# Kernel tuning notes

Hardware: AMD Instinct MI355X
Metric: run time of the kernel (lower is better)

Reference implementation:

```python
import jax, jax.numpy as jnp
import numpy as np

NEG_SLOPE = 0.2  # PyG GATConv default negative_slope


def gat_conv(x, edge_index, W, a_src, a_dst, b):
    """PyG GATConv with add_self_loops=True, concat=False (mean over heads).
    x: [N, F_in]; W: [F_in, H*D]; a_src/a_dst: [H, D]; b: [D].
    Returns [N, D].
    """
    N = x.shape[0]
    H, D = a_src.shape
    xh = (x @ W).reshape(N, H, D)            # [N, H, D]
    loop = jnp.arange(N, dtype=edge_index.dtype)
    src = jnp.concatenate([edge_index[0], loop])  # [E+N]
    dst = jnp.concatenate([edge_index[1], loop])  # [E+N]
    # per-node attention logits
    asrc = jnp.einsum('nhd,hd->nh', xh, a_src)    # [N, H]
    adst = jnp.einsum('nhd,hd->nh', xh, a_dst)    # [N, H]
    e = asrc[src] + adst[dst]                      # [E+N, H]
    e = jnp.where(e > 0, e, NEG_SLOPE * e)         # LeakyReLU
    # softmax over incoming edges of each destination node
    emax = jax.ops.segment_max(e, dst, num_segments=N)   # [N, H]
    ex = jnp.exp(e - emax[dst])
    denom = jax.ops.segment_sum(ex, dst, num_segments=N) # [N, H]
    alpha = ex / denom[dst]                               # [E+N, H]
    # scatter-aggregate messages
    out = jax.ops.segment_sum(alpha[:, :, None] * xh[src], dst, num_segments=N)  # [N, H, D]
    return out.mean(axis=1) + b                           # concat=False -> mean heads


def setup_inputs() -> dict:
    key = jax.random.key(0)
    ks = jax.random.split(key, 10)
    N, F, D, C, H, E = 100000, 128, 32, 16, 8, 1600000
    s1 = 1.0 / np.sqrt(F)
    s2 = 1.0 / np.sqrt(D)
    return {
        'x': jax.random.normal(ks[0], (N, F), dtype=jnp.float32),
        'edge_index': jax.random.randint(ks[1], (2, E), 0, N, dtype=jnp.int32),
        'W1': jax.random.normal(ks[2], (F, H * D), dtype=jnp.float32) * s1,
        'a_src1': jax.random.normal(ks[3], (H, D), dtype=jnp.float32) * s2,
        'a_dst1': jax.random.normal(ks[4], (H, D), dtype=jnp.float32) * s2,
        'b1': jnp.zeros((D,), dtype=jnp.float32),
        'W2': jax.random.normal(ks[5], (D, H * C), dtype=jnp.float32) * s2,
        'a_src2': jax.random.normal(ks[6], (H, C), dtype=jnp.float32) * (1.0 / np.sqrt(C)),
        'a_dst2': jax.random.normal(ks[7], (H, C), dtype=jnp.float32) * (1.0 / np.sqrt(C)),
        'b2': jnp.zeros((C,), dtype=jnp.float32),
    }


def reference(x, edge_index, W1, a_src1, a_dst1, b1, W2, a_src2, a_dst2, b2):
    h = gat_conv(x, edge_index, W1, a_src1, a_dst1, b1)
    h = jax.nn.elu(h)                       # F.elu; Dropout(p=0.0) is identity
    logits = gat_conv(h, edge_index, W2, a_src2, a_dst2, b2)
    return (jax.nn.log_softmax(logits, axis=1), logits)
```

## Files before the change

### kernel.cpp

```cpp
#include <hip/hip_runtime.h>
#include <hip/hip_bf16.h>
#include <hip/hip_fp16.h>
#include <math.h>

#define LEAK 0.2f
#define BSTRIDE 64
#define NPB 128
#define CAPB 4096

typedef _Float16 f16;
typedef _Float16 f16x8 __attribute__((ext_vector_type(8)));
typedef float f32x2 __attribute__((ext_vector_type(2)));
typedef float f32x4 __attribute__((ext_vector_type(4)));

__global__ void transpose_w_k(const float* __restrict__ W, f16* __restrict__ Wt,
                              int K, int NC) {
  int idx = blockIdx.x * 256 + threadIdx.x;
  if (idx >= K * NC) return;
  int n = idx / K, k = idx - n * K;
  Wt[idx] = (f16)W[(size_t)k * NC + n];
}

__global__ __launch_bounds__(256) void binscatter_k(const int* __restrict__ ei, int E,
                                                    int Nn,
                                                    unsigned* __restrict__ binCnt,
                                                    uint2* __restrict__ recs, int NB) {
  __shared__ unsigned lh[1024];
  __shared__ unsigned gbase[1024];
  const int Mtot = E + Nn;
  for (int i = threadIdx.x; i < NB; i += 256) lh[i] = 0;
  __syncthreads();
  const int base = blockIdx.x * 4096;
  int sr[16], dr[16];
#pragma unroll
  for (int j = 0; j < 16; ++j) {
    int p = base + j * 256 + threadIdx.x;
    if (p < Mtot) {
      int ss, dd;
      if (p < E) {
        ss = ei[p];
        dd = ei[E + p];
      } else {
        ss = dd = p - E;
      }
      sr[j] = ss;
      dr[j] = dd;
      atomicAdd(&lh[dd >> 7], 1u);
    } else {
      dr[j] = -1;
      sr[j] = 0;
    }
  }
  __syncthreads();
  for (int i = threadIdx.x; i < NB; i += 256) {
    unsigned c = lh[i];
    gbase[i] = c ? atomicAdd(&binCnt[i], c) : 0u;
    lh[i] = 0;
  }
  __syncthreads();
#pragma unroll
  for (int j = 0; j < 16; ++j) {
    if (dr[j] >= 0) {
      int b = dr[j] >> 7;
      unsigned pos = gbase[b] + atomicAdd(&lh[b], 1u);
      if (pos < CAPB)
        recs[((size_t)b << 12) + pos] = make_uint2((unsigned)sr[j], (unsigned)dr[j]);
    }
  }
}

__global__ __launch_bounds__(256) void binbuild_k(const uint2* __restrict__ recs,
                                                  const unsigned* __restrict__ binCnt,
                                                  unsigned* __restrict__ cnt,
                                                  unsigned* __restrict__ bucket, int N) {
  __shared__ unsigned lcnt[NPB];
  __shared__ unsigned lbkt[NPB * BSTRIDE];
  const int b = blockIdx.x;
  for (int i = threadIdx.x; i < NPB; i += 256) lcnt[i] = 0;
  __syncthreads();
  unsigned nrec = binCnt[b];
  nrec = nrec > CAPB ? CAPB : nrec;
  const unsigned r0 = (unsigned)b << 12;
  const unsigned r1 = r0 + nrec;
  for (unsigned p = r0 + threadIdx.x; p < r1; p += 256) {
    uint2 r = recs[p];
    unsigned dl = r.y & (NPB - 1);
    unsigned pos = atomicAdd(&lcnt[dl], 1u);
    if (pos < BSTRIDE) lbkt[(dl << 6) + pos] = r.x;
  }
  __syncthreads();
  const int n0 = b * NPB;
  const int nv = (N - n0) < NPB ? (N - n0) : NPB;
  for (int i = threadIdx.x; i < nv; i += 256) cnt[n0 + i] = lcnt[i];
  uint4* gb = (uint4*)(bucket + ((size_t)n0 << 6));
  const uint4* lb = (const uint4*)lbkt;
  const int lim = nv * (BSTRIDE / 4);
  for (int i = threadIdx.x; i < lim; i += 256) gb[i] = lb[i];
}

template <int K, int BN, int DH>
__global__ __launch_bounds__(256) void gemm_att_mfma_k(
    const float* __restrict__ A, const f16* __restrict__ Bt,
    unsigned char* __restrict__ Cout, const float* __restrict__ a_src,
    const float* __restrict__ a_dst, float* __restrict__ asrc,
    float* __restrict__ adst, int M, int NC) {
  constexpr int CH = K / 8;
  constexpr int CT = BN / 16;
  constexpr int KT = K / 32;
  constexpr int LDSB = (BN * K * 2) > (64 * BN) ? (BN * K * 2) : (64 * BN);
  __shared__ __align__(16) unsigned char smem[LDSB];
  f16* Bs = (f16*)smem;
  unsigned char* stage = smem;
  const int tid = threadIdx.x;
  const int row0 = blockIdx.y * 64;
  const int col0 = blockIdx.x * BN;

#pragma unroll
  for (int it = 0; it < (BN * CH) / 256; ++it) {
    int idx = it * 256 + tid;
    int n = idx / CH, c = idx - n * CH;
    f16x8 h = *(const f16x8*)(Bt + (size_t)(col0 + n) * K + c * 8);
    *(f16x8*)&Bs[n * K + (((c + n) & (CH - 1)) << 3)] = h;
  }

  const int wv = tid >> 6;
  const int lane = tid & 63;
  const int l16 = lane & 15;
  const int l4 = lane >> 4;

  const int arow = row0 + wv * 16 + l16;
  const bool aok = arow < M;
  f16x8 afrag[KT];
#pragma unroll
  for (int kt = 0; kt < KT; ++kt) {
    float4 v0 = make_float4(0.f, 0.f, 0.f, 0.f), v1 = v0;
    if (aok) {
      const float* gp = A + (size_t)arow * K + (kt * 4 + l4) * 8;
      v0 = *(const float4*)gp;
      v1 = *(const float4*)(gp + 4);
    }
    afrag[kt] = {(f16)v0.x, (f16)v0.y, (f16)v0.z, (f16)v0.w,
                 (f16)v1.x, (f16)v1.y, (f16)v1.z, (f16)v1.w};
  }
  __syncthreads();

  f32x4 acc[CT];
#pragma unroll
  for (int ct = 0; ct < CT; ++ct) acc[ct] = (f32x4){0.f, 0.f, 0.f, 0.f};

#pragma unroll
  for (int kt = 0; kt < KT; ++kt) {
    int aj = kt * 4 + l4;
#pragma unroll
    for (int ct = 0; ct < CT; ++ct) {
      int br = ct * 16 + l16;
      f16x8 bv = *(const f16x8*)&Bs[br * K + (((aj + br) & (CH - 1)) << 3)];
      acc[ct] = __builtin_amdgcn_mfma_f32_16x16x32_f16(afrag[kt], bv, acc[ct], 0, 0, 0);
    }
  }

  constexpr int HPB = BN / DH;
  constexpr int CTH = DH / 16;
  float ps[HPB][4], pd[HPB][4];
#pragma unroll
  for (int hl = 0; hl < HPB; ++hl)
#pragma unroll
    for (int r = 0; r < 4; ++r) { ps[hl][r] = 0.f; pd[hl][r] = 0.f; }

#pragma unroll
  for (int ct = 0; ct < CT; ++ct) {
    int col = col0 + ct * 16 + l16;
    float vs = a_src[col];
    float vd = a_dst[col];
    int hl = ct / CTH;
#pragma unroll
    for (int r = 0; r < 4; ++r) {
      ps[hl][r] += acc[ct][r] * vs;
      pd[hl][r] += acc[ct][r] * vd;
    }
  }

#pragma unroll
  for (int hl = 0; hl < HPB; ++hl) {
#pragma unroll
    for (int r = 0; r < 4; ++r) {
      float s = ps[hl][r], d = pd[hl][r];
#pragma unroll
      for (int m = 1; m < 16; m <<= 1) {
        s += __shfl_xor(s, m, 64);
        d += __shfl_xor(d, m, 64);
      }
      if (l16 == 0) {
        int grow = row0 + wv * 16 + l4 * 4 + r;
        int h = (col0 / DH) + hl;
        if (grow < M) {
          asrc[(size_t)grow * 8 + h] = s;
          adst[(size_t)grow * 8 + h] = d;
        }
      }
    }
  }

  __syncthreads();
  {
    const int j = lane & 3;
    const unsigned selAB = ((4u + j) << (8 * j)) | ((unsigned)j << (8 * (j ^ 1)));
    const unsigned selCD = ((4u + j) << (8 * (j ^ 2))) | ((unsigned)j << (8 * (j ^ 3)));
    const unsigned selMix =
        0x03020100u + (0x04040404u & ((j & 2) ? 0xFFFF0000u : 0x0000FFFFu));
    const int row = wv * 16 + l4 * 4 + j;
    const int colq = (l16 >> 2) * 4;
    const int swz = (row & 7) << 4;
#pragma unroll
    for (int ct = 0; ct < CT; ++ct) {
      unsigned wpk = (unsigned)__builtin_amdgcn_cvt_pk_fp8_f32(
          acc[ct][0], acc[ct][1], 0, false);
      wpk = (unsigned)__builtin_amdgcn_cvt_pk_fp8_f32(
          acc[ct][2], acc[ct][3], (int)wpk, true);
      unsigned Bx = (unsigned)__shfl_xor((int)wpk, 1, 64);
      unsigned Cx = (unsigned)__shfl_xor((int)wpk, 2, 64);
      unsigned Dx = (unsigned)__shfl_xor((int)wpk, 3, 64);
      unsigned P1 = __builtin_amdgcn_perm(wpk, Bx, selAB);
      unsigned P2 = __builtin_amdgcn_perm(Cx, Dx, selCD);
      unsigned ow = __builtin_amdgcn_perm(P1, P2, selMix);
      int colb = ct * 16 + colq;
      *(unsigned*)&stage[row * BN + (colb ^ swz)] = ow;
    }
  }
  __syncthreads();
  {
    constexpr int CPR = BN / 16;
#pragma unroll
    for (int i = 0; i < (64 * CPR) / 256; ++i) {
      int cid = i * 256 + tid;
      int row = cid / CPR, ch = cid - row * CPR;
      int grow = row0 + row;
      if (grow < M) {
        uint4 v = *(const uint4*)&stage[row * BN + ((ch * 16) ^ ((row & 7) << 4))];
        *(uint4*)(Cout + (size_t)grow * NC + col0 + ch * 16) = v;
      }
    }
  }
}

__global__ __launch_bounds__(256) void aggregate1_k(const unsigned char* __restrict__ xh8,
                                                    const float* __restrict__ asrc,
                                                    const float* __restrict__ adst,
                                                    const unsigned* __restrict__ cnt,
                                                    const unsigned* __restrict__ bucket,
                                                    const float* __restrict__ b1,
                                                    float* __restrict__ hout, int N) {
  __shared__ float wlds[4][64][8];
  __shared__ unsigned slds[4][64];
  const int lane = threadIdx.x & 63;
  const int wv = threadIdx.x >> 6;
  const int n = blockIdx.x * 4 + wv;
  const int nn = n < N ? n : N - 1;
  int deg = (int)cnt[nn];
  deg = deg > BSTRIDE ? BSTRIDE : deg;
  unsigned sv = bucket[((size_t)nn << 6) + lane];
  if (lane >= deg) sv = 0;

  float w[8];
  if (lane < deg) {
    const float4* ap = (const float4*)(asrc + (size_t)sv * 8);
    const float4* bp = (const float4*)(adst + (size_t)nn * 8);
    float4 a0 = ap[0], a1 = ap[1];
    float4 b0 = bp[0], b1v = bp[1];
    float e[8] = {a0.x + b0.x, a0.y + b0.y, a0.z + b0.z, a0.w + b0.w,
                  a1.x + b1v.x, a1.y + b1v.y, a1.z + b1v.z, a1.w + b1v.w};
#pragma unroll
    for (int j = 0; j < 8; ++j) {
      float t = e[j];
      t = t > 0.f ? t : LEAK * t;
      w[j] = __expf(t);
    }
  } else {
#pragma unroll
    for (int j = 0; j < 8; ++j) w[j] = 0.f;
  }
  *(float4*)&wlds[wv][lane][0] = make_float4(w[0], w[1], w[2], w[3]);
  *(float4*)&wlds[wv][lane][4] = make_float4(w[4], w[5], w[6], w[7]);
  slds[wv][lane] = sv;
  __syncthreads();
  if (n >= N) return;

  const int sub = lane >> 5;
  const int sl = lane & 31;
  const int h = sl >> 2;
  const uint2* xw = (const uint2*)xh8;

  float a0 = 0.f, a1 = 0.f, a2 = 0.f, a3 = 0.f;
  float a4 = 0.f, a5 = 0.f, a6 = 0.f, a7 = 0.f;
  float dsum = 0.f;
#pragma unroll 4
  for (int i = 0; i < deg; i += 2) {
    float w8 = wlds[wv][i + sub][h];
    unsigned s = slds[wv][i + sub];
    uint2 b = xw[(size_t)s * 32 + sl];
    f32x2 p0 = __builtin_amdgcn_cvt_pk_f32_fp8(b.x, false);
    f32x2 p1 = __builtin_amdgcn_cvt_pk_f32_fp8(b.x, true);
    f32x2 p2 = __builtin_amdgcn_cvt_pk_f32_fp8(b.y, false);
    f32x2 p3 = __builtin_amdgcn_cvt_pk_f32_fp8(b.y, true);
    a0 += w8 * p0.x; a1 += w8 * p0.y; a2 += w8 * p1.x; a3 += w8 * p1.y;
    a4 += w8 * p2.x; a5 += w8 * p2.y; a6 += w8 * p3.x; a7 += w8 * p3.y;
    dsum += w8;
  }

  a0 += __shfl_xor(a0, 32, 64); a1 += __shfl_xor(a1, 32, 64);
  a2 += __shfl_xor(a2, 32, 64); a3 += __shfl_xor(a3, 32, 64);
  a4 += __shfl_xor(a4, 32, 64); a5 += __shfl_xor(a5, 32, 64);
  a6 += __shfl_xor(a6, 32, 64); a7 += __shfl_xor(a7, 32, 64);
  dsum += __shfl_xor(dsum, 32, 64);

  float rinv = 0.125f * __builtin_amdgcn_rcpf(dsum);
  a0 *= rinv; a1 *= rinv; a2 *= rinv; a3 *= rinv;
  a4 *= rinv; a5 *= rinv; a6 *= rinv; a7 *= rinv;

#pragma unroll
  for (int m = 16; m >= 4; m >>= 1) {
    a0 += __shfl_xor(a0, m, 64); a1 += __shfl_xor(a1, m, 64);
    a2 += __shfl_xor(a2, m, 64); a3 += __shfl_xor(a3, m, 64);
    a4 += __shfl_xor(a4, m, 64); a5 += __shfl_xor(a5, m, 64);
    a6 += __shfl_xor(a6, m, 64); a7 += __shfl_xor(a7, m, 64);
  }
  if (lane < 4) {
    int d = lane * 8;
    float4 bv0 = *(const float4*)(b1 + d);
    float4 bv1 = *(const float4*)(b1 + d + 4);
    float o0 = a0 + bv0.x, o1 = a1 + bv0.y, o2 = a2 + bv0.z, o3 = a3 + bv0.w;
    float o4 = a4 + bv1.x, o5 = a5 + bv1.y, o6 = a6 + bv1.z, o7 = a7 + bv1.w;
    o0 = o0 > 0.f ? o0 : expm1f(o0);
    o1 = o1 > 0.f ? o1 : expm1f(o1);
    o2 = o2 > 0.f ? o2 : expm1f(o2);
    o3 = o3 > 0.f ? o3 : expm1f(o3);
    o4 = o4 > 0.f ? o4 : expm1f(o4);
    o5 = o5 > 0.f ? o5 : expm1f(o5);
    o6 = o6 > 0.f ? o6 : expm1f(o6);
    o7 = o7 > 0.f ? o7 : expm1f(o7);
    *(float4*)(hout + (size_t)n * 32 + d) = make_float4(o0, o1, o2, o3);
    *(float4*)(hout + (size_t)n * 32 + d + 4) = make_float4(o4, o5, o6, o7);
  }
}

__global__ __launch_bounds__(256) void aggregate2_k(const unsigned char* __restrict__ xq,
                                                    const float* __restrict__ asrc,
                                                    const float* __restrict__ adst,
                                                    const unsigned* __restrict__ cnt,
                                                    const unsigned* __restrict__ bucket,
                                                    const float* __restrict__ b2,
                                                    float* __restrict__ out, int N) {
  __shared__ float wlds[4][64][8];
  __shared__ unsigned slds[4][64];
  const int lane = threadIdx.x & 63;
  const int wv = threadIdx.x >> 6;
  const int n = blockIdx.x * 4 + wv;
  const int nn = n < N ? n : N - 1;
  int deg = (int)cnt[nn];
  deg = deg > BSTRIDE ? BSTRIDE : deg;
  unsigned sv = bucket[((size_t)nn << 6) + lane];
  if (lane >= deg) sv = 0;

  float w[8];
  if (lane < deg) {
    const float4* ap = (const float4*)(asrc + (size_t)sv * 8);
    const float4* bp = (const float4*)(adst + (size_t)nn * 8);
    float4 a0 = ap[0], a1 = ap[1];
    float4 b0 = bp[0], b1v = bp[1];
    float e[8] = {a0.x + b0.x, a0.y + b0.y, a0.z + b0.z, a0.w + b0.w,
                  a1.x + b1v.x, a1.y + b1v.y, a1.z + b1v.z, a1.w + b1v.w};
#pragma unroll
    for (int j = 0; j < 8; ++j) {
      float t = e[j];
      t = t > 0.f ? t : LEAK * t;
      w[j] = __expf(t);
    }
  } else {
#pragma unroll
    for (int j = 0; j < 8; ++j) w[j] = 0.f;
  }
  *(float4*)&wlds[wv][lane][0] = make_float4(w[0], w[1], w[2], w[3]);
  *(float4*)&wlds[wv][lane][4] = make_float4(w[4], w[5], w[6], w[7]);
  slds[wv][lane] = sv;
  __syncthreads();
  if (n >= N) return;

  const int sub = lane >> 5;
  const int sl = lane & 31;
  const int h = sl >> 2;
  const unsigned* xw = (const unsigned*)xq;

  float a0 = 0.f, a1 = 0.f, a2 = 0.f, a3 = 0.f;
  float dsum = 0.f;
#pragma unroll 4
  for (int i = 0; i < deg; i += 2) {
    float w8 = wlds[wv][i + sub][h];
    unsigned s = slds[wv][i + sub];
    unsigned b = xw[(size_t)s * 32 + sl];
    f32x2 p0 = __builtin_amdgcn_cvt_pk_f32_fp8(b, false);
    f32x2 p1 = __builtin_amdgcn_cvt_pk_f32_fp8(b, true);
    a0 += w8 * p0.x; a1 += w8 * p0.y; a2 += w8 * p1.x; a3 += w8 * p1.y;
    dsum += w8;
  }

  a0 += __shfl_xor(a0, 32, 64); a1 += __shfl_xor(a1, 32, 64);
  a2 += __shfl_xor(a2, 32, 64); a3 += __shfl_xor(a3, 32, 64);
  dsum += __shfl_xor(dsum, 32, 64);

  float rinv = 0.125f * __builtin_amdgcn_rcpf(dsum);
  a0 *= rinv; a1 *= rinv; a2 *= rinv; a3 *= rinv;

#pragma unroll
  for (int m = 16; m >= 4; m >>= 1) {
    a0 += __shfl_xor(a0, m, 64); a1 += __shfl_xor(a1, m, 64);
    a2 += __shfl_xor(a2, m, 64); a3 += __shfl_xor(a3, m, 64);
  }
  int c = (lane & 3) * 4;
  float4 bv = *(const float4*)(b2 + c);
  float l0 = a0 + bv.x, l1 = a1 + bv.y, l2 = a2 + bv.z, l3 = a3 + bv.w;

  float mx = fmaxf(fmaxf(l0, l1), fmaxf(l2, l3));
  mx = fmaxf(mx, __shfl_xor(mx, 1, 64));
  mx = fmaxf(mx, __shfl_xor(mx, 2, 64));
  float es = __expf(l0 - mx) + __expf(l1 - mx) + __expf(l2 - mx) + __expf(l3 - mx);
  es += __shfl_xor(es, 1, 64);
  es += __shfl_xor(es, 2, 64);
  float lse = logf(es) + mx;

  if (lane < 4) {
    *(float4*)(out + (size_t)n * 16 + c) = make_float4(l0 - lse, l1 - lse, l2 - lse, l3 - lse);
    *(float4*)(out + (size_t)N * 16 + (size_t)n * 16 + c) = make_float4(l0, l1, l2, l3);
  }
}

extern "C" void kernel_launch(void* const* d_in, const int* in_sizes, int n_in,
                              void* d_out, int out_size, void* d_ws, size_t ws_size,
                              hipStream_t stream) {
  const float* x      = (const float*)d_in[0];
  const int*   ei     = (const int*)d_in[1];
  const float* W1     = (const float*)d_in[2];
  const float* a_src1 = (const float*)d_in[3];
  const float* a_dst1 = (const float*)d_in[4];
  const float* b1     = (const float*)d_in[5];
  const float* W2     = (const float*)d_in[6];
  const float* a_src2 = (const float*)d_in[7];
  const float* a_dst2 = (const float*)d_in[8];
  const float* b2     = (const float*)d_in[9];

  const int N = in_sizes[0] / 128;
  const int E = in_sizes[1] / 2;
  const int Mtot = E + N;
  const int NB = (N + NPB - 1) / NPB;

  char* w = (char*)d_ws;
  size_t used = 0;
  auto alloc = [&](size_t bytes) -> void* {
    size_t aligned = (bytes + 255) & ~(size_t)255;
    void* p = w + used;
    used += aligned;
    return p;
  };
  unsigned char* xh1q = (unsigned char*)alloc((size_t)N * 256);
  unsigned char* xh2q = xh1q;
  float*    hbuf   = (float*)alloc((size_t)N * 32 * 4);
  float*    asrc   = (float*)alloc((size_t)N * 8 * 4);
  float*    adst   = (float*)alloc((size_t)N * 8 * 4);
  unsigned* cnt    = (unsigned*)alloc((size_t)N * 4);
  unsigned* bucket = (unsigned*)alloc((size_t)N * BSTRIDE * 4);
  f16*      w1t    = (f16*)alloc((size_t)128 * 256 * 2);
  f16*      w2t    = (f16*)alloc((size_t)32 * 128 * 2);
  uint2*    recs   = (uint2*)alloc((size_t)NB * CAPB * 8);
  unsigned* binCnt = (unsigned*)alloc((size_t)NB * 4);
  (void)ws_size;

  float* out = (float*)d_out;
  const int gy = (N + 63) / 64;
  const int nchunk = (Mtot + 4095) / 4096;

  hipMemsetAsync(binCnt, 0, (size_t)NB * 4, stream);
  transpose_w_k<<<(128 * 256 + 255) / 256, 256, 0, stream>>>(W1, w1t, 128, 256);
  transpose_w_k<<<(32 * 128 + 255) / 256, 256, 0, stream>>>(W2, w2t, 32, 128);

  binscatter_k<<<nchunk, 256, 0, stream>>>(ei, E, N, binCnt, recs, NB);
  binbuild_k<<<NB, 256, 0, stream>>>(recs, binCnt, cnt, bucket, N);

  gemm_att_mfma_k<128, 128, 32><<<dim3(2, gy), 256, 0, stream>>>(
      x, w1t, xh1q, a_src1, a_dst1, asrc, adst, N, 256);

  aggregate1_k<<<(N + 3) / 4, 256, 0, stream>>>(xh1q, asrc, adst, cnt, bucket, b1, hbuf, N);

  gemm_att_mfma_k<32, 128, 16><<<dim3(1, gy), 256, 0, stream>>>(
      hbuf, w2t, xh2q, a_src2, a_dst2, asrc, adst, N, 128);
  aggregate2_k<<<(N + 3) / 4, 256, 0, stream>>>(xh2q, asrc, adst, cnt, bucket, b2, out, N);
}
```

Measured before the change: 355.2 us.

## Fuse edge binning scatter into first GEMM kernel epilogue

Moves the edge bin-scatter pass into the tail of the first GEMM+attention kernel. Each GEMM block now bins a 2048-edge chunk, reusing its shared memory, which removes one kernel launch and lets the scatter's memory traffic overlap with GEMM work on other blocks. It also switches the aggregate2 bucket loads and output stores to nontemporal hints. The fused kernel uses more registers and shared memory, which may lower occupancy, and it only covers the edges if there are enough GEMM blocks (3126 blocks × 2048 ≥ 1.7M edges holds here).

```diff
diff --git a/kernel.cpp b/kernel.cpp
--- a/kernel.cpp
+++ b/kernel.cpp
@@ -19,54 +19,6 @@
   if (idx >= K * NC) return;
   int n = idx / K, k = idx - n * K;
   Wt[idx] = (f16)W[(size_t)k * NC + n];
-}
-
-__global__ __launch_bounds__(256) void binscatter_k(const int* __restrict__ ei, int E,
-                                                    int Nn,
-                                                    unsigned* __restrict__ binCnt,
-                                                    uint2* __restrict__ recs, int NB) {
-  __shared__ unsigned lh[1024];
-  __shared__ unsigned gbase[1024];
-  const int Mtot = E + Nn;
-  for (int i = threadIdx.x; i < NB; i += 256) lh[i] = 0;
-  __syncthreads();
-  const int base = blockIdx.x * 4096;
-  int sr[16], dr[16];
-#pragma unroll
-  for (int j = 0; j < 16; ++j) {
-    int p = base + j * 256 + threadIdx.x;
-    if (p < Mtot) {
-      int ss, dd;
-      if (p < E) {
-        ss = ei[p];
-        dd = ei[E + p];
-      } else {
-        ss = dd = p - E;
-      }
-      sr[j] = ss;
-      dr[j] = dd;
-      atomicAdd(&lh[dd >> 7], 1u);
-    } else {
-      dr[j] = -1;
-      sr[j] = 0;
-    }
-  }
-  __syncthreads();
-  for (int i = threadIdx.x; i < NB; i += 256) {
-    unsigned c = lh[i];
-    gbase[i] = c ? atomicAdd(&binCnt[i], c) : 0u;
-    lh[i] = 0;
-  }
-  __syncthreads();
-#pragma unroll
-  for (int j = 0; j < 16; ++j) {
-    if (dr[j] >= 0) {
-      int b = dr[j] >> 7;
-      unsigned pos = gbase[b] + atomicAdd(&lh[b], 1u);
-      if (pos < CAPB)
-        recs[((size_t)b << 12) + pos] = make_uint2((unsigned)sr[j], (unsigned)dr[j]);
-    }
-  }
 }
 
 __global__ __launch_bounds__(256) void binbuild_k(const uint2* __restrict__ recs,
@@ -98,12 +50,15 @@
   for (int i = threadIdx.x; i < lim; i += 256) gb[i] = lb[i];
 }
 
-template <int K, int BN, int DH>
+template <int K, int BN, int DH, bool FILL>
 __global__ __launch_bounds__(256) void gemm_att_mfma_k(
     const float* __restrict__ A, const f16* __restrict__ Bt,
     unsigned char* __restrict__ Cout, const float* __restrict__ a_src,
     const float* __restrict__ a_dst, float* __restrict__ asrc,
-    float* __restrict__ adst, int M, int NC) {
+    float* __restrict__ adst, int M, int NC,
+    const int* __restrict__ ei, int E, int Nn,
+    unsigned* __restrict__ binCnt, unsigned long long* __restrict__ recs,
+    int NB) {
   constexpr int CH = K / 8;
   constexpr int CT = BN / 16;
   constexpr int KT = K / 32;
@@ -238,6 +193,58 @@
       if (grow < M) {
         uint4 v = *(const uint4*)&stage[row * BN + ((ch * 16) ^ ((row & 7) << 4))];
         *(uint4*)(Cout + (size_t)grow * NC + col0 + ch * 16) = v;
+      }
+    }
+  }
+
+  if (FILL) {
+    __syncthreads();
+    unsigned* lh = (unsigned*)smem;
+    unsigned* gb2 = ((unsigned*)smem) + 1024;
+    const int chunk = (int)(blockIdx.y * gridDim.x + blockIdx.x);
+    const int Mtot = E + Nn;
+    const int base = chunk * 2048;
+    if (base < Mtot) {
+      for (int i = tid; i < NB; i += 256) lh[i] = 0;
+      __syncthreads();
+      int sr[8], dr[8];
+#pragma unroll
+      for (int j = 0; j < 8; ++j) {
+        int p = base + j * 256 + tid;
+        if (p < Mtot) {
+          int ss, dd;
+          if (p < E) {
+            ss = ei[p];
+            dd = ei[E + p];
+          } else {
+            ss = dd = p - E;
+          }
+          sr[j] = ss;
+          dr[j] = dd;
+          atomicAdd(&lh[dd >> 7], 1u);
+        } else {
+          dr[j] = -1;
+          sr[j] = 0;
+        }
+      }
+      __syncthreads();
+      for (int i = tid; i < NB; i += 256) {
+        unsigned c = lh[i];
+        gb2[i] = c ? atomicAdd(&binCnt[i], c) : 0u;
+        lh[i] = 0;
+      }
+      __syncthreads();
+#pragma unroll
+      for (int j = 0; j < 8; ++j) {
+        if (dr[j] >= 0) {
+          int b = dr[j] >> 7;
+          unsigned pos = gb2[b] + atomicAdd(&lh[b], 1u);
+          if (pos < CAPB) {
+            unsigned long long rec =
+                ((unsigned long long)(unsigned)dr[j] << 32) | (unsigned)sr[j];
+            recs[((size_t)b << 12) + pos] = rec;
+          }
+        }
       }
     }
   }
@@ -358,7 +365,7 @@
   const int nn = n < N ? n : N - 1;
   int deg = (int)cnt[nn];
   deg = deg > BSTRIDE ? BSTRIDE : deg;
-  unsigned sv = bucket[((size_t)nn << 6) + lane];
+  unsigned sv = __builtin_nontemporal_load(&bucket[((size_t)nn << 6) + lane]);
   if (lane >= deg) sv = 0;
 
   float w[8];
@@ -428,8 +435,10 @@
   float lse = logf(es) + mx;
 
   if (lane < 4) {
-    *(float4*)(out + (size_t)n * 16 + c) = make_float4(l0 - lse, l1 - lse, l2 - lse, l3 - lse);
-    *(float4*)(out + (size_t)N * 16 + (size_t)n * 16 + c) = make_float4(l0, l1, l2, l3);
+    f32x4 v0 = {l0 - lse, l1 - lse, l2 - lse, l3 - lse};
+    f32x4 v1 = {l0, l1, l2, l3};
+    __builtin_nontemporal_store(v0, (f32x4*)(out + (size_t)n * 16 + c));
+    __builtin_nontemporal_store(v1, (f32x4*)(out + (size_t)N * 16 + (size_t)n * 16 + c));
   }
 }
 
@@ -469,27 +478,27 @@
   unsigned* bucket = (unsigned*)alloc((size_t)N * BSTRIDE * 4);
   f16*      w1t    = (f16*)alloc((size_t)128 * 256 * 2);
   f16*      w2t    = (f16*)alloc((size_t)32 * 128 * 2);
-  uint2*    recs   = (uint2*)alloc((size_t)NB * CAPB * 8);
+  unsigned long long* recs = (unsigned long long*)alloc((size_t)NB * CAPB * 8);
   unsigned* binCnt = (unsigned*)alloc((size_t)NB * 4);
   (void)ws_size;
 
   float* out = (float*)d_out;
   const int gy = (N + 63) / 64;
-  const int nchunk = (Mtot + 4095) / 4096;
 
   hipMemsetAsync(binCnt, 0, (size_t)NB * 4, stream);
   transpose_w_k<<<(128 * 256 + 255) / 256, 256, 0, stream>>>(W1, w1t, 128, 256);
   transpose_w_k<<<(32 * 128 + 255) / 256, 256, 0, stream>>>(W2, w2t, 32, 128);
 
-  binscatter_k<<<nchunk, 256, 0, stream>>>(ei, E, N, binCnt, recs, NB);
-  binbuild_k<<<NB, 256, 0, stream>>>(recs, binCnt, cnt, bucket, N);
-
-  gemm_att_mfma_k<128, 128, 32><<<dim3(2, gy), 256, 0, stream>>>(
-      x, w1t, xh1q, a_src1, a_dst1, asrc, adst, N, 256);
+  gemm_att_mfma_k<128, 128, 32, true><<<dim3(2, gy), 256, 0, stream>>>(
+      x, w1t, xh1q, a_src1, a_dst1, asrc, adst, N, 256,
+      ei, E, N, binCnt, recs, NB);
+
+  binbuild_k<<<NB, 256, 0, stream>>>((const uint2*)recs, binCnt, cnt, bucket, N);
 
   aggregate1_k<<<(N + 3) / 4, 256, 0, stream>>>(xh1q, asrc, adst, cnt, bucket, b1, hbuf, N);
 
-  gemm_att_mfma_k<32, 128, 16><<<dim3(1, gy), 256, 0, stream>>>(
-      hbuf, w2t, xh2q, a_src2, a_dst2, asrc, adst, N, 128);
+  gemm_att_mfma_k<32, 128, 16, false><<<dim3(1, gy), 256, 0, stream>>>(
+      hbuf, w2t, xh2q, a_src2, a_dst2, asrc, adst, N, 128,
+      nullptr, 0, 0, nullptr, nullptr, 0);
   aggregate2_k<<<(N + 3) / 4, 256, 0, stream>>>(xh2q, asrc, adst, cnt, bucket, b2, out, N);
 }
```

After: 348.4 us. No clear change (-1.9%).
